# Kernel tuning notes

Hardware: AMD Instinct MI355X
Metric: run time of the kernel (lower is better)

The kernel has to match this reference:

```python
import jax, jax.numpy as jnp
import numpy as np

N = 100000      # nodes
E = 1600000     # edges (avg degree 16)
G = 1024        # graphs in the batch
D_IN = 128      # input_size
D_EMB = 128     # embedding_size


def _l2_normalize(x, eps=1e-12):
    # F.normalize(p=2, dim=-1): x / max(||x||_2, eps)
    n = jnp.sqrt(jnp.sum(x * x, axis=-1, keepdims=True))
    return x / jnp.maximum(n, eps)


def setup_inputs() -> dict:
    key = jax.random.key(0)
    ks = jax.random.split(key, 11)
    x = jax.random.normal(ks[0], (N, D_IN), dtype=jnp.float32)
    edge_src = jax.random.randint(ks[1], (E,), 0, N, dtype=jnp.int32)
    edge_dst = jax.random.randint(ks[2], (E,), 0, N, dtype=jnp.int32)
    edge_val = jax.random.uniform(ks[3], (E,), dtype=jnp.float32)  # normalized adjacency weights
    batch_ids = jax.random.randint(ks[4], (N,), 0, G, dtype=jnp.int32)
    batch_val = jax.random.uniform(ks[5], (N,), dtype=jnp.float32)  # pooling weights
    # parameters (xavier-ish scales)
    lim_in = float(np.sqrt(6.0 / (D_IN + D_EMB)))
    lim_e = float(np.sqrt(6.0 / (D_EMB + D_EMB)))
    W_in = jax.random.uniform(ks[6], (D_IN, D_EMB), minval=-lim_in, maxval=lim_in, dtype=jnp.float32)
    b_in = jnp.zeros((D_EMB,), dtype=jnp.float32)
    W_gcn = jax.random.uniform(ks[7], (D_EMB, D_EMB), minval=-lim_e, maxval=lim_e, dtype=jnp.float32)
    W_g = jax.random.uniform(ks[8], (D_EMB, D_EMB), minval=-lim_e, maxval=lim_e, dtype=jnp.float32)
    b_g = jnp.zeros((D_EMB,), dtype=jnp.float32)
    return dict(x=x, edge_src=edge_src, edge_dst=edge_dst, edge_val=edge_val,
                batch_ids=batch_ids, batch_val=batch_val,
                W_in=W_in, b_in=b_in, W_gcn=W_gcn, W_g=W_g, b_g=b_g,
                num_nodes=N, num_graphs=G)


def reference(x, edge_src, edge_dst, edge_val, batch_ids, batch_val,
              W_in, b_in, W_gcn, W_g, b_g, num_nodes, num_graphs):
    # h = relu(fc_input(x))                          [N, D_EMB]
    h = jax.nn.relu(x @ W_in + b_in)
    # h_struct = sparse.mm(A, h) @ W_gcn ; A in COO: out[i] = sum_e val[e]*h[dst[e]] for src[e]==i
    msgs = h[edge_dst] * edge_val[:, None]           # [E, D_EMB]
    agg = jax.ops.segment_sum(msgs, edge_src, num_segments=num_nodes)
    h_struct = _l2_normalize(jax.nn.relu(agg @ W_gcn))
    # h_graph = sparse.mm(B, h_struct): weighted pool of nodes into graphs
    h_graph = jax.ops.segment_sum(h_struct * batch_val[:, None], batch_ids, num_segments=num_graphs)
    h_graph = _l2_normalize(jax.nn.relu(h_graph @ W_g + b_g))
    return (h_struct, h_graph)
```

## Files before the change

kernel.cpp:

```cpp
#include <hip/hip_runtime.h>
#include <hip/hip_bf16.h>

#define D 128
#define GCAP 192
#define NBKT 8

typedef __attribute__((ext_vector_type(8))) short short8;
typedef __attribute__((ext_vector_type(4))) float f32x4;

__device__ __forceinline__ float b2f(unsigned short u) {
    union { unsigned int i; float f; } v;
    v.i = ((unsigned int)u) << 16;
    return v.f;
}
__device__ __forceinline__ unsigned short f2b(float f) {
    __hip_bfloat16 h = __float2bfloat16(f);
    return __builtin_bit_cast(unsigned short, h);
}

__global__ void k_prep(const float* __restrict__ Wa, unsigned short* __restrict__ Ahi,
                       unsigned short* __restrict__ Alo,
                       const float* __restrict__ Wb, unsigned short* __restrict__ Bhi,
                       unsigned short* __restrict__ Blo) {
    int b = blockIdx.x;
    const float* W = (b < 64) ? Wa : Wb;
    unsigned short* Hi = (b < 64) ? Ahi : Bhi;
    unsigned short* Lo = (b < 64) ? Alo : Blo;
    int i = (b & 63) * 256 + threadIdx.x;
    int k = i >> 7, n = i & 127;
    float w = W[i];
    unsigned short hi = f2b(w);
    unsigned short lo = f2b(w - b2f(hi));
    Hi[n * D + k] = hi;
    Lo[n * D + k] = lo;
}

__global__ __launch_bounds__(256) void k_part(
        const int* __restrict__ esrc, const int* __restrict__ edst,
        const float* __restrict__ eval,
        int* __restrict__ cnt, int* __restrict__ bcur,
        int2* __restrict__ bdv, int* __restrict__ bsrc,
        int bucketCap, int NR, int E,
        const int* __restrict__ bids, const float* __restrict__ bval,
        int* __restrict__ gcnt, int2* __restrict__ gdata, int N) {
    __shared__ int lcnt[NBKT];
    __shared__ int lbase[NBKT];
    const int tid = threadIdx.x;
    const int i = blockIdx.x * 256 + tid;

    if (tid < NBKT) lcnt[tid] = 0;
    __syncthreads();

    int s = 0, bkt = 0, my = 0;
    if (i < E) {
        s = esrc[i];
        bkt = s / NR;
        my = atomicAdd(&lcnt[bkt], 1);
        atomicAdd(&cnt[s], 1);
    }
    __syncthreads();
    if (tid < NBKT) lbase[tid] = atomicAdd(&bcur[tid], lcnt[tid]);
    __syncthreads();

    if (i < E) {
        int slot = lbase[bkt] + my;
        if (slot < bucketCap) {
            size_t idx = (size_t)bkt * bucketCap + slot;
            int2 d; d.x = edst[i]; d.y = __float_as_int(eval[i]);
            bdv[idx] = d;
            bsrc[idx] = s;
        }
    }

    if (i < N) {
        int g = bids[i];
        int slot = atomicAdd(&gcnt[g], 1);
        if (slot < GCAP) {
            int2 d; d.x = i; d.y = __float_as_int(bval[i]);
            gdata[(size_t)g * GCAP + slot] = d;
        }
    }
}

__global__ __launch_bounds__(256) void k_scan1(
        const int* __restrict__ cnt, int* __restrict__ tmp,
        int* __restrict__ bsum, int N) {
    __shared__ int s[256];
    int tid = threadIdx.x;
    int i = blockIdx.x * 256 + tid;
    int v = (i < N) ? cnt[i] : 0;
    s[tid] = v; __syncthreads();
#pragma unroll
    for (int d = 1; d < 256; d <<= 1) {
        int a = (tid >= d) ? s[tid - d] : 0;
        __syncthreads();
        s[tid] += a;
        __syncthreads();
    }
    if (i < N) tmp[i] = s[tid] - v;
    if (tid == 255) bsum[blockIdx.x] = s[255];
}

__global__ __launch_bounds__(256) void k_scan2(int* __restrict__ bsum, int B1) {
    __shared__ int s[256];
    int tid = threadIdx.x;
    int base = 0;
    for (int t0 = 0; t0 < B1; t0 += 256) {
        int i = t0 + tid;
        int v = (i < B1) ? bsum[i] : 0;
        s[tid] = v; __syncthreads();
#pragma unroll
        for (int d = 1; d < 256; d <<= 1) {
            int a = (tid >= d) ? s[tid - d] : 0;
            __syncthreads();
            s[tid] += a;
            __syncthreads();
        }
        if (i < B1) bsum[i] = base + s[tid] - v;
        int tot = s[255];
        __syncthreads();
        base += tot;
    }
}

__global__ __launch_bounds__(256) void k_scan3(
        const int* __restrict__ tmp, const int* __restrict__ bsum,
        int* __restrict__ offs, int* __restrict__ cursor, int N, int E) {
    int i = blockIdx.x * 256 + threadIdx.x;
    if (i < N) {
        int o = tmp[i] + bsum[i >> 8];
        offs[i] = o;
        cursor[i] = o;
    }
    if (i == 0) offs[N] = E;
}

__global__ __launch_bounds__(256) void k_scatter2(
        const int* __restrict__ bcur,
        const int2* __restrict__ bdv, const int* __restrict__ bsrc,
        int* __restrict__ cursor, int2* __restrict__ edata, int bucketCap) {
    const int grp = blockIdx.x & 7;
    const int bi = blockIdx.x >> 3;
    const int stride = (gridDim.x >> 3) * 256;
    int nrec = bcur[grp];
    if (nrec > bucketCap) nrec = bucketCap;
    const size_t base = (size_t)grp * bucketCap;

    for (int j = bi * 256 + threadIdx.x; j < nrec; j += stride) {
        int s = bsrc[base + j];
        int2 dv = bdv[base + j];
        int slot = atomicAdd(&cursor[s], 1);
        edata[slot] = dv;
    }
}

__global__ __launch_bounds__(256, 3) void k_gemm_fused(
        const float* __restrict__ X,
        const unsigned short* __restrict__ W1hi, const unsigned short* __restrict__ W1lo,
        const float* __restrict__ bias1,
        const unsigned short* __restrict__ W2hi, const unsigned short* __restrict__ W2lo,
        unsigned short* __restrict__ HW, int N) {
    __shared__ __align__(16) char wbuf[2][16384];
    __shared__ float htile_s[4 * 16 * 68];
    const int tid  = threadIdx.x;
    const int wave = tid >> 6;
    const int lane = tid & 63;
    const int q = lane >> 4;
    const int l15 = lane & 15;
    const int lane16 = lane * 16;
    const int row0 = blockIdx.x * 64 + wave * 16;
    float* tile = htile_s + wave * 16 * 68;

    int arow = row0 + l15;
    if (arow >= N) arow = N - 1;
    const float* xrow = X + (size_t)arow * D;

    uint4 r0, r1, r2, r3;
#define LOAD_WCHUNK(Whi, Wlo, kkc)                                              \
    {                                                                           \
        int s0 = tid, s1 = tid + 256;                                           \
        int t0_ = s0 >> 6, q0_ = (s0 >> 4) & 3, l0_ = s0 & 15;                  \
        int t1_ = s1 >> 6, q1_ = (s1 >> 4) & 3, l1_ = s1 & 15;                  \
        size_t g0 = (size_t)(t0_ * 16 + l0_) * 256 + (kkc) * 64 + q0_ * 16;     \
        size_t g1 = (size_t)(t1_ * 16 + l1_) * 256 + (kkc) * 64 + q1_ * 16;     \
        r0 = *(const uint4*)((const char*)(Whi) + g0);                          \
        r1 = *(const uint4*)((const char*)(Whi) + g1);                          \
        r2 = *(const uint4*)((const char*)(Wlo) + g0);                          \
        r3 = *(const uint4*)((const char*)(Wlo) + g1);                          \
    }
#define STORE_WCHUNK(buf)                                                       \
    {                                                                           \
        ((uint4*)(buf))[tid] = r0;                                              \
        ((uint4*)(buf))[tid + 256] = r1;                                        \
        ((uint4*)((buf) + 8192))[tid] = r2;                                     \
        ((uint4*)((buf) + 8192))[tid + 256] = r3;                               \
    }

    LOAD_WCHUNK(W1hi, W1lo, 0);

    short8 xhi[4], xlo[4];
#pragma unroll
    for (int kk = 0; kk < 4; kk++) {
        float4 f0 = *(const float4*)(xrow + kk * 32 + q * 8);
        float4 f1 = *(const float4*)(xrow + kk * 32 + q * 8 + 4);
        float fv[8] = {f0.x, f0.y, f0.z, f0.w, f1.x, f1.y, f1.z, f1.w};
#pragma unroll
        for (int j = 0; j < 8; j++) {
            unsigned short h = f2b(fv[j]);
            xhi[kk][j] = (short)h;
            xlo[kk][j] = (short)f2b(fv[j] - b2f(h));
        }
    }

    STORE_WCHUNK(wbuf[0]);

    f32x4 acc[8];
#pragma unroll
    for (int t = 0; t < 8; t++) acc[t] = (f32x4){0.f, 0.f, 0.f, 0.f};

#pragma unroll
    for (int kk = 0; kk < 4; kk++) {
        __syncthreads();
        if (kk < 3) { LOAD_WCHUNK(W1hi, W1lo, kk + 1); }
        else        { LOAD_WCHUNK(W2hi, W2lo, 0); }
        const char* cb = wbuf[kk & 1];
#pragma unroll
        for (int t = 0; t < 8; t++) {
            short8 bhi = *(const short8*)(cb + t * 1024 + lane16);
            short8 blo = *(const short8*)(cb + 8192 + t * 1024 + lane16);
            acc[t] = __builtin_amdgcn_mfma_f32_16x16x32_bf16(xhi[kk], bhi, acc[t], 0, 0, 0);
            acc[t] = __builtin_amdgcn_mfma_f32_16x16x32_bf16(xhi[kk], blo, acc[t], 0, 0, 0);
            acc[t] = __builtin_amdgcn_mfma_f32_16x16x32_bf16(xlo[kk], bhi, acc[t], 0, 0, 0);
        }
        STORE_WCHUNK(wbuf[(kk + 1) & 1]);
    }

    f32x4 acc2[8];
#pragma unroll
    for (int t = 0; t < 8; t++) acc2[t] = (f32x4){0.f, 0.f, 0.f, 0.f};

#pragma unroll
    for (int hf = 0; hf < 2; hf++) {
#pragma unroll
        for (int tt = 0; tt < 4; tt++) {
            int t = hf * 4 + tt;
            int col = t * 16 + l15;
            float bv = bias1[col];
#pragma unroll
            for (int rr = 0; rr < 4; rr++) {
                float v = acc[t][rr] + bv;
                v = v > 0.f ? v : 0.f;
                tile[(q * 4 + rr) * 68 + tt * 16 + l15] = v;
            }
        }
#pragma unroll
        for (int kk2 = 0; kk2 < 2; kk2++) {
            int c = hf * 2 + kk2;
            __syncthreads();
            if (c < 3) { LOAD_WCHUNK(W2hi, W2lo, c + 1); }
            const float* hp = tile + l15 * 68 + kk2 * 32 + q * 8;
            float4 f0 = *(const float4*)(hp);
            float4 f1 = *(const float4*)(hp + 4);
            float fv[8] = {f0.x, f0.y, f0.z, f0.w, f1.x, f1.y, f1.z, f1.w};
            short8 ahi, alo;
#pragma unroll
            for (int j = 0; j < 8; j++) {
                unsigned short h = f2b(fv[j]);
                ahi[j] = (short)h;
                alo[j] = (short)f2b(fv[j] - b2f(h));
            }
            const char* cb = wbuf[c & 1];
#pragma unroll
            for (int t2 = 0; t2 < 8; t2++) {
                short8 bhi = *(const short8*)(cb + t2 * 1024 + lane16);
                short8 blo = *(const short8*)(cb + 8192 + t2 * 1024 + lane16);
                acc2[t2] = __builtin_amdgcn_mfma_f32_16x16x32_bf16(ahi, bhi, acc2[t2], 0, 0, 0);
                acc2[t2] = __builtin_amdgcn_mfma_f32_16x16x32_bf16(ahi, blo, acc2[t2], 0, 0, 0);
                acc2[t2] = __builtin_amdgcn_mfma_f32_16x16x32_bf16(alo, bhi, acc2[t2], 0, 0, 0);
            }
            if (c < 3) { STORE_WCHUNK(wbuf[(c + 1) & 1]); }
        }
    }

#pragma unroll
    for (int t = 0; t < 8; t++) {
        int col = t * 16 + l15;
#pragma unroll
        for (int rr = 0; rr < 4; rr++) {
            int row = row0 + q * 4 + rr;
            if (row < N) HW[(size_t)row * D + col] = f2b(acc2[t][rr]);
        }
    }
#undef LOAD_WCHUNK
#undef STORE_WCHUNK
}

__global__ __launch_bounds__(256) void k_agg_finalize(
        const int* __restrict__ offs, const int2* __restrict__ edata,
        const unsigned int* __restrict__ hw32,
        float* __restrict__ hstruct, int N) {
    const int lane = threadIdx.x & 63;
    const int node = blockIdx.x * 4 + (threadIdx.x >> 6);
    if (node >= N) return;
    int base0 = offs[node];
    int deg = offs[node + 1] - base0;

    float a0 = 0.f, a1 = 0.f;
    for (int b = 0; b < deg; b += 64) {
        int nrem = deg - b; if (nrem > 64) nrem = 64;
        int myDst = 0; float myVal = 0.f;
        if (lane < nrem) {
            int2 ed = edata[base0 + b + lane];
            myDst = ed.x; myVal = __int_as_float(ed.y);
        }
#pragma unroll 4
        for (int j = 0; j < nrem; j++) {
            int dj = __shfl(myDst, j, 64);
            float vj = __shfl(myVal, j, 64);
            unsigned int p = hw32[(size_t)dj * 64 + lane];
            a0 = fmaf(vj, b2f((unsigned short)(p & 0xffffu)), a0);
            a1 = fmaf(vj, b2f((unsigned short)(p >> 16)), a1);
        }
    }

    a0 = a0 > 0.f ? a0 : 0.f;
    a1 = a1 > 0.f ? a1 : 0.f;
    float ss = a0 * a0 + a1 * a1;
#pragma unroll
    for (int m = 1; m < 64; m <<= 1) ss += __shfl_xor(ss, m, 64);
    float scale = 1.0f / fmaxf(sqrtf(ss), 1e-12f);
    float2 o; o.x = a0 * scale; o.y = a1 * scale;
    *(float2*)(hstruct + (size_t)node * D + 2 * lane) = o;
}

__global__ __launch_bounds__(256) void k_graph_finalize(
        const int* __restrict__ gcnt, const int2* __restrict__ gdata,
        const float* __restrict__ hstruct,
        const float* __restrict__ Wg, const float* __restrict__ bg,
        float* __restrict__ out, int G) {
    __shared__ float part[4][128];
    __shared__ float part2[4][128];
    const int lane = threadIdx.x & 63;
    const int wave = threadIdx.x >> 6;
    const int g = blockIdx.x;
    if (g >= G) return;
    const int c0 = 2 * lane;

    int deg = gcnt[g];
    if (deg > GCAP) deg = GCAP;

    float a0 = 0.f, a1 = 0.f;
    int cw = (deg > wave) ? ((deg - wave + 3) >> 2) : 0;
    for (int base = 0; base < cw; base += 64) {
        int nrem = cw - base; if (nrem > 64) nrem = 64;
        int myNode = 0; float myW = 0.f;
        if (lane < nrem) {
            int idx = (base + lane) * 4 + wave;
            int2 ed = gdata[(size_t)g * GCAP + idx];
            myNode = ed.x; myW = __int_as_float(ed.y);
        }
#pragma unroll 4
        for (int j = 0; j < nrem; j++) {
            int nj = __shfl(myNode, j, 64);
            float wj = __shfl(myW, j, 64);
            float2 hs = *(const float2*)(hstruct + (size_t)nj * D + c0);
            a0 = fmaf(wj, hs.x, a0);
            a1 = fmaf(wj, hs.y, a1);
        }
    }
    part[wave][c0]     = a0;
    part[wave][c0 + 1] = a1;
    __syncthreads();
    a0 = part[0][c0]     + part[1][c0]     + part[2][c0]     + part[3][c0];
    a1 = part[0][c0 + 1] + part[1][c0 + 1] + part[2][c0 + 1] + part[3][c0 + 1];

    float o0 = 0.f, o1 = 0.f;
#pragma unroll 2
    for (int kq = 0; kq < 32; kq++) {
        int k = wave * 32 + kq;
        float xv = (k & 1) ? __shfl(a1, k >> 1, 64) : __shfl(a0, k >> 1, 64);
        float2 w = *(const float2*)(Wg + (size_t)k * D + c0);
        o0 = fmaf(xv, w.x, o0);
        o1 = fmaf(xv, w.y, o1);
    }
    part2[wave][c0]     = o0;
    part2[wave][c0 + 1] = o1;
    __syncthreads();
    if (wave == 0) {
        o0 = part2[0][c0]     + part2[1][c0]     + part2[2][c0]     + part2[3][c0];
        o1 = part2[0][c0 + 1] + part2[1][c0 + 1] + part2[2][c0 + 1] + part2[3][c0 + 1];
        o0 += bg[c0];
        o1 += bg[c0 + 1];
        o0 = o0 > 0.f ? o0 : 0.f;
        o1 = o1 > 0.f ? o1 : 0.f;
        float ss = o0 * o0 + o1 * o1;
#pragma unroll
        for (int m = 1; m < 64; m <<= 1) ss += __shfl_xor(ss, m, 64);
        float scale = 1.0f / fmaxf(sqrtf(ss), 1e-12f);
        float2 o; o.x = o0 * scale; o.y = o1 * scale;
        *(float2*)(out + (size_t)g * D + c0) = o;
    }
}

extern "C" void kernel_launch(void* const* d_in, const int* in_sizes, int n_in,
                              void* d_out, int out_size, void* d_ws, size_t ws_size,
                              hipStream_t stream) {
    const float* x     = (const float*)d_in[0];
    const int*   esrc  = (const int*)d_in[1];
    const int*   edst  = (const int*)d_in[2];
    const float* eval  = (const float*)d_in[3];
    const int*   bids  = (const int*)d_in[4];
    const float* bval  = (const float*)d_in[5];
    const float* W_in  = (const float*)d_in[6];
    const float* b_in  = (const float*)d_in[7];
    const float* W_gcn = (const float*)d_in[8];
    const float* W_g   = (const float*)d_in[9];
    const float* b_g   = (const float*)d_in[10];

    const int N = in_sizes[4];
    const int E = in_sizes[1];
    const int G = 1024;

    const int B1 = (N + 255) / 256;
    const int NR = (N + NBKT - 1) / NBKT;
    const int bucketCap = E / NBKT + E / 64;

    auto pad = [](size_t v) { return (v + 255) & ~(size_t)255; };
    char* ws = (char*)d_ws;
    unsigned short* whi_in  = (unsigned short*)ws; ws += pad((size_t)D * D * 2);
    unsigned short* wlo_in  = (unsigned short*)ws; ws += pad((size_t)D * D * 2);
    unsigned short* whi_gcn = (unsigned short*)ws; ws += pad((size_t)D * D * 2);
    unsigned short* wlo_gcn = (unsigned short*)ws; ws += pad((size_t)D * D * 2);
    int*   cnt    = (int*)ws;  ws += pad((size_t)N * 4);
    int*   gcnt   = (int*)ws;  ws += pad((size_t)G * 4);
    int*   bcur   = (int*)ws;  ws += pad((size_t)NBKT * 4);
    int*   tmp    = (int*)ws;  ws += pad((size_t)N * 4);
    int*   bsum   = (int*)ws;  ws += pad((size_t)B1 * 4);
    int*   offs   = (int*)ws;  ws += pad((size_t)(N + 1) * 4);
    int*   cursor = (int*)ws;  ws += pad((size_t)N * 4);
    unsigned short* hw = (unsigned short*)ws; ws += pad((size_t)N * D * 2);
    int2*  edata  = (int2*)ws; ws += pad((size_t)E * 8);
    int2*  gdata  = (int2*)ws; ws += pad((size_t)G * GCAP * 8);
    int2*  bdv    = (int2*)ws; ws += pad((size_t)NBKT * bucketCap * 8);
    int*   bsrc   = (int*)ws;  ws += pad((size_t)NBKT * bucketCap * 4);

    hipMemsetAsync(cnt, 0, (size_t)((char*)bcur - (char*)cnt) + pad((size_t)NBKT * 4), stream);

    k_prep<<<128, 256, 0, stream>>>(W_in, whi_in, wlo_in, W_gcn, whi_gcn, wlo_gcn);

    int mb = ((E > N ? E : N) + 255) / 256;
    k_part<<<mb, 256, 0, stream>>>(esrc, edst, eval, cnt, bcur, bdv, bsrc,
                                   bucketCap, NR, E, bids, bval, gcnt, gdata, N);
    k_scan1<<<B1, 256, 0, stream>>>(cnt, tmp, bsum, N);
    k_scan2<<<1, 256, 0, stream>>>(bsum, B1);
    k_scan3<<<B1, 256, 0, stream>>>(tmp, bsum, offs, cursor, N, E);
    k_scatter2<<<2048, 256, 0, stream>>>(bcur, bdv, bsrc, cursor, edata, bucketCap);

    const int gb = (N + 63) / 64;
    k_gemm_fused<<<gb, 256, 0, stream>>>(x, whi_in, wlo_in, b_in,
                                         whi_gcn, wlo_gcn, hw, N);

    float* hstruct = (float*)d_out;
    float* hgraph  = hstruct + (size_t)N * D;

    k_agg_finalize<<<(N + 3) / 4, 256, 0, stream>>>(offs, edata,
                                                    (const unsigned int*)hw, hstruct, N);
    k_graph_finalize<<<G, 256, 0, stream>>>(gcnt, gdata, hstruct, W_g, b_g, hgraph, G);
}
```

Baseline: 469.9 us.

## Stage bucketed edges in LDS and write contiguous interleaved records

The partition kernel now handles 512 edges per block. It first sorts them by bucket in shared memory, then writes each bucket's run contiguously as interleaved (dst, val, src) triples instead of scattered int2 plus separate int arrays. The scatter pass reads the matching 12-byte records. The aim is better write coalescing and fewer separate streams in the partition step, at the cost of more LDS use and extra barriers.

```diff
diff --git a/kernel.cpp b/kernel.cpp
--- a/kernel.cpp
+++ b/kernel.cpp
@@ -4,6 +4,7 @@
 #define D 128
 #define GCAP 192
 #define NBKT 8
+#define EPB 512
 
 typedef __attribute__((ext_vector_type(8))) short short8;
 typedef __attribute__((ext_vector_type(4))) float f32x4;
@@ -39,44 +40,83 @@
         const int* __restrict__ esrc, const int* __restrict__ edst,
         const float* __restrict__ eval,
         int* __restrict__ cnt, int* __restrict__ bcur,
-        int2* __restrict__ bdv, int* __restrict__ bsrc,
+        int* __restrict__ brec,
         int bucketCap, int NR, int E,
         const int* __restrict__ bids, const float* __restrict__ bval,
         int* __restrict__ gcnt, int2* __restrict__ gdata, int N) {
     __shared__ int lcnt[NBKT];
+    __shared__ int lofs[NBKT];
     __shared__ int lbase[NBKT];
+    __shared__ int ltot;
+    __shared__ int ssrc[EPB], sdst[EPB], sval[EPB];
+    __shared__ unsigned char sbkt[EPB];
     const int tid = threadIdx.x;
-    const int i = blockIdx.x * 256 + tid;
+    const int i0 = blockIdx.x * EPB + tid;
+    const int i1 = i0 + 256;
 
     if (tid < NBKT) lcnt[tid] = 0;
     __syncthreads();
 
-    int s = 0, bkt = 0, my = 0;
-    if (i < E) {
-        s = esrc[i];
-        bkt = s / NR;
-        my = atomicAdd(&lcnt[bkt], 1);
-        atomicAdd(&cnt[s], 1);
+    int s0 = 0, d0 = 0, v0 = 0, b0 = 0, m0 = -1;
+    int s1 = 0, d1 = 0, v1 = 0, b1 = 0, m1 = -1;
+    if (i0 < E) {
+        s0 = esrc[i0]; d0 = edst[i0]; v0 = __float_as_int(eval[i0]);
+        b0 = s0 / NR;
+        m0 = atomicAdd(&lcnt[b0], 1);
+        atomicAdd(&cnt[s0], 1);
+    }
+    if (i1 < E) {
+        s1 = esrc[i1]; d1 = edst[i1]; v1 = __float_as_int(eval[i1]);
+        b1 = s1 / NR;
+        m1 = atomicAdd(&lcnt[b1], 1);
+        atomicAdd(&cnt[s1], 1);
     }
     __syncthreads();
+
+    if (tid == 0) {
+        int run = 0;
+#pragma unroll
+        for (int b = 0; b < NBKT; b++) { lofs[b] = run; run += lcnt[b]; }
+        ltot = run;
+    }
     if (tid < NBKT) lbase[tid] = atomicAdd(&bcur[tid], lcnt[tid]);
     __syncthreads();
 
-    if (i < E) {
-        int slot = lbase[bkt] + my;
+    if (m0 >= 0) {
+        int p = lofs[b0] + m0;
+        ssrc[p] = s0; sdst[p] = d0; sval[p] = v0; sbkt[p] = (unsigned char)b0;
+    }
+    if (m1 >= 0) {
+        int p = lofs[b1] + m1;
+        ssrc[p] = s1; sdst[p] = d1; sval[p] = v1; sbkt[p] = (unsigned char)b1;
+    }
+    __syncthreads();
+
+    int total = ltot;
+    for (int t = tid; t < total; t += 256) {
+        int b = sbkt[t];
+        int slot = lbase[b] + (t - lofs[b]);
         if (slot < bucketCap) {
-            size_t idx = (size_t)bkt * bucketCap + slot;
-            int2 d; d.x = edst[i]; d.y = __float_as_int(eval[i]);
-            bdv[idx] = d;
-            bsrc[idx] = s;
-        }
-    }
-
-    if (i < N) {
-        int g = bids[i];
+            size_t w = ((size_t)b * bucketCap + slot) * 3;
+            brec[w]     = sdst[t];
+            brec[w + 1] = sval[t];
+            brec[w + 2] = ssrc[t];
+        }
+    }
+
+    if (i0 < N) {
+        int g = bids[i0];
         int slot = atomicAdd(&gcnt[g], 1);
         if (slot < GCAP) {
-            int2 d; d.x = i; d.y = __float_as_int(bval[i]);
+            int2 d; d.x = i0; d.y = __float_as_int(bval[i0]);
+            gdata[(size_t)g * GCAP + slot] = d;
+        }
+    }
+    if (i1 < N) {
+        int g = bids[i1];
+        int slot = atomicAdd(&gcnt[g], 1);
+        if (slot < GCAP) {
+            int2 d; d.x = i1; d.y = __float_as_int(bval[i1]);
             gdata[(size_t)g * GCAP + slot] = d;
         }
     }
@@ -136,8 +176,7 @@
 }
 
 __global__ __launch_bounds__(256) void k_scatter2(
-        const int* __restrict__ bcur,
-        const int2* __restrict__ bdv, const int* __restrict__ bsrc,
+        const int* __restrict__ bcur, const int* __restrict__ brec,
         int* __restrict__ cursor, int2* __restrict__ edata, int bucketCap) {
     const int grp = blockIdx.x & 7;
     const int bi = blockIdx.x >> 3;
@@ -147,9 +186,12 @@
     const size_t base = (size_t)grp * bucketCap;
 
     for (int j = bi * 256 + threadIdx.x; j < nrec; j += stride) {
-        int s = bsrc[base + j];
-        int2 dv = bdv[base + j];
+        size_t w = (base + j) * 3;
+        int dst = brec[w];
+        int val = brec[w + 1];
+        int s   = brec[w + 2];
         int slot = atomicAdd(&cursor[s], 1);
+        int2 dv; dv.x = dst; dv.y = val;
         edata[slot] = dv;
     }
 }
@@ -441,20 +483,19 @@
     unsigned short* hw = (unsigned short*)ws; ws += pad((size_t)N * D * 2);
     int2*  edata  = (int2*)ws; ws += pad((size_t)E * 8);
     int2*  gdata  = (int2*)ws; ws += pad((size_t)G * GCAP * 8);
-    int2*  bdv    = (int2*)ws; ws += pad((size_t)NBKT * bucketCap * 8);
-    int*   bsrc   = (int*)ws;  ws += pad((size_t)NBKT * bucketCap * 4);
+    int*   brec   = (int*)ws;  ws += pad((size_t)NBKT * bucketCap * 12);
 
     hipMemsetAsync(cnt, 0, (size_t)((char*)bcur - (char*)cnt) + pad((size_t)NBKT * 4), stream);
 
     k_prep<<<128, 256, 0, stream>>>(W_in, whi_in, wlo_in, W_gcn, whi_gcn, wlo_gcn);
 
-    int mb = ((E > N ? E : N) + 255) / 256;
-    k_part<<<mb, 256, 0, stream>>>(esrc, edst, eval, cnt, bcur, bdv, bsrc,
+    int mb = ((E > N ? E : N) + EPB - 1) / EPB;
+    k_part<<<mb, 256, 0, stream>>>(esrc, edst, eval, cnt, bcur, brec,
                                    bucketCap, NR, E, bids, bval, gcnt, gdata, N);
     k_scan1<<<B1, 256, 0, stream>>>(cnt, tmp, bsum, N);
     k_scan2<<<1, 256, 0, stream>>>(bsum, B1);
     k_scan3<<<B1, 256, 0, stream>>>(tmp, bsum, offs, cursor, N, E);
-    k_scatter2<<<2048, 256, 0, stream>>>(bcur, bdv, bsrc, cursor, edata, bucketCap);
+    k_scatter2<<<2048, 256, 0, stream>>>(bcur, brec, cursor, edata, bucketCap);
 
     const int gb = (N + 63) / 64;
     k_gemm_fused<<<gb, 256, 0, stream>>>(x, whi_in, wlo_in, b_in,
```

New measurement: 445.1 us. 5.3% less time.
